# Kernel optimization log

Measured on AMD Instinct MI355X. Metric: run time of the kernel, lower is better.

The kernel has to match this reference:

```python
import jax, jax.numpy as jnp
import numpy as np

N = 50000      # total nodes
E = 800000     # total edges
IN = 8         # in_channels
H = 16         # hidden_dim
OUT = 16       # out_channels
B = 64         # number of graphs in batch


def _glorot(k, shape):
    fan_out, fan_in = shape[0], shape[1]
    lim = float(np.sqrt(6.0 / (fan_in + fan_out)))
    return jax.random.uniform(k, shape, jnp.float32, -lim, lim)


def setup_inputs() -> dict:
    key = jax.random.key(0)
    ks = jax.random.split(key, 12)
    return {
        "x": jax.random.normal(ks[0], (N, IN), jnp.float32),
        "edge_attr": jax.random.uniform(ks[1], (E, 1), jnp.float32),
        # edge MLP 1: Linear(1, H) -> ReLU -> Linear(H, IN*H)
        "W_e1a": _glorot(ks[2], (H, 1)), "b_e1a": jnp.zeros((H,), jnp.float32),
        "W_e1b": _glorot(ks[3], (IN * H, H)), "b_e1b": jnp.zeros((IN * H,), jnp.float32),
        "root1": _glorot(ks[4], (IN, H)), "bias1": jnp.zeros((H,), jnp.float32),
        # edge MLP 2: Linear(1, H) -> ReLU -> Linear(H, H*OUT)
        "W_e2a": _glorot(ks[5], (H, 1)), "b_e2a": jnp.zeros((H,), jnp.float32),
        "W_e2b": _glorot(ks[6], (H * OUT, H)), "b_e2b": jnp.zeros((H * OUT,), jnp.float32),
        "root2": _glorot(ks[7], (H, OUT)), "bias2": jnp.zeros((OUT,), jnp.float32),
        "edge_index": jax.random.randint(ks[8], (2, E), 0, N, jnp.int32),
        "batch": jnp.sort(jax.random.randint(ks[9], (N,), 0, B, jnp.int32)),
    }


def _segment_mean(vals, idx, num_segments):
    s = jax.ops.segment_sum(vals, idx, num_segments=num_segments)
    cnt = jax.ops.segment_sum(jnp.ones((vals.shape[0],), vals.dtype), idx,
                              num_segments=num_segments)
    return s / jnp.maximum(cnt, 1.0)[:, None]


def _nnconv(x, src, dst, edge_attr, Wa, ba, Wb, bb, root, bias, din, dout):
    # edge MLP -> per-edge weight matrix [E, din, dout]
    he = jax.nn.relu(edge_attr @ Wa.T + ba)
    We = (he @ Wb.T + bb).reshape(-1, din, dout)
    # per-edge matmul on gathered source features, scatter-mean to dst
    msg = jnp.einsum('ei,eio->eo', x[src], We)
    agg = _segment_mean(msg, dst, x.shape[0])
    return agg + x @ root + bias


def reference(x, edge_attr, W_e1a, b_e1a, W_e1b, b_e1b, root1, bias1,
              W_e2a, b_e2a, W_e2b, b_e2b, root2, bias2, edge_index, batch):
    src, dst = edge_index[0], edge_index[1]
    h = jax.nn.relu(_nnconv(x, src, dst, edge_attr,
                            W_e1a, b_e1a, W_e1b, b_e1b, root1, bias1, IN, H))
    h = jax.nn.relu(_nnconv(h, src, dst, edge_attr,
                            W_e2a, b_e2a, W_e2b, b_e2b, root2, bias2, H, OUT))
    g = _segment_mean(h, batch, B)  # global mean pool per graph
    return (h, g, batch)
```

## Files before the change

### kernel.cpp

```cpp
#include <hip/hip_runtime.h>
#include <hip/hip_bf16.h>

typedef __bf16 bf16;
typedef __bf16 bf16x8 __attribute__((ext_vector_type(8)));
typedef float  f32x4  __attribute__((ext_vector_type(4)));


__global__ void node_pre1(const float* __restrict__ x,
                          const float* __restrict__ b_e1b,
                          const float* __restrict__ root1,
                          const float* __restrict__ bias1,
                          float* __restrict__ d1, float* __restrict__ r1, int N)
{
    int t = blockIdx.x * blockDim.x + threadIdx.x;
    int v = t >> 4, o = t & 15;
    if (v >= N) return;
    float dacc = 0.f, racc = 0.f;
#pragma unroll
    for (int i = 0; i < 8; ++i) {
        float xv = x[v * 8 + i];
        dacc += xv * b_e1b[i * 16 + o];
        racc += xv * root1[i * 16 + o];
    }
    d1[v * 16 + o] = dacc;
    r1[v * 16 + o] = racc + bias1[o];
}

__global__ void edge_l1(const float* __restrict__ x,
                        const float* __restrict__ ea,
                        const int*   __restrict__ eidx,
                        const float* __restrict__ W_e1a, const float* __restrict__ b_e1a,
                        const float* __restrict__ W_e1b,
                        const float* __restrict__ d1,
                        float* __restrict__ agg, int* __restrict__ cnt,
                        int E, int ntiles)
{
    const int lane = threadIdx.x & 63;
    const int m = lane & 15;
    const int q = lane >> 4;
    const int wave   = blockIdx.x * (blockDim.x >> 6) + (threadIdx.x >> 6);
    const int nwaves = gridDim.x * (blockDim.x >> 6);

    bf16x8 bfrag[4];
#pragma unroll
    for (int c = 0; c < 4; ++c)
#pragma unroll
        for (int t = 0; t < 8; ++t)
            bfrag[c][t] = (bf16)W_e1b[(t * 16 + m) * 16 + (c * 4 + q)];

    float wa[4], bb[4];
#pragma unroll
    for (int c = 0; c < 4; ++c) { wa[c] = W_e1a[c * 4 + q]; bb[c] = b_e1a[c * 4 + q]; }

    int tile = wave;
    if (tile >= ntiles) return;

    int e = tile * 16 + m;
    int s = eidx[e];
    int d = eidx[E + e];
    float t_ea = ea[e];

    while (tile < ntiles) {
        const int ntile = tile + nwaves;
        int s_nx = s, d_nx = d; float ea_nx = t_ea;
        if (ntile < ntiles) {
            int en = ntile * 16 + m;
            s_nx  = eidx[en];
            d_nx  = eidx[E + en];
            ea_nx = ea[en];
        }

        const float4* xp = (const float4*)(x + (size_t)s * 8);
        float4 x0 = xp[0], x1 = xp[1];

        int d_r[4];
        f32x4 acc;
#pragma unroll
        for (int reg = 0; reg < 4; ++reg) {
            int r = q * 4 + reg;
            int s_r = __shfl(s, r, 64);
            d_r[reg] = __shfl(d, r, 64);
            acc[reg] = d1[s_r * 16 + m];
        }

        float he[4];
#pragma unroll
        for (int c = 0; c < 4; ++c) {
            float h = wa[c] * t_ea + bb[c];
            he[c] = h > 0.f ? h : 0.f;
        }

        float xv[8] = {x0.x, x0.y, x0.z, x0.w, x1.x, x1.y, x1.z, x1.w};
#pragma unroll
        for (int c = 0; c < 4; ++c) {
            bf16x8 afrag;
#pragma unroll
            for (int t = 0; t < 8; ++t) afrag[t] = (bf16)(he[c] * xv[t]);
            acc = __builtin_amdgcn_mfma_f32_16x16x32_bf16(afrag, bfrag[c], acc, 0, 0, 0);
        }

        if (q == 0) atomicAdd(&cnt[d], 1);

#pragma unroll
        for (int reg = 0; reg < 4; ++reg)
            atomicAdd(&agg[d_r[reg] * 16 + m], acc[reg]);

        s = s_nx; d = d_nx; t_ea = ea_nx; tile = ntile;
    }
}

__global__ void node_fin1(const float* __restrict__ agg, const int* __restrict__ cnt,
                          const float* __restrict__ r1,
                          const float* __restrict__ b_e2b, const float* __restrict__ root2,
                          const float* __restrict__ bias2,
                          float* __restrict__ h1, float* __restrict__ d2,
                          float* __restrict__ r2, int N)
{
    int t = blockIdx.x * blockDim.x + threadIdx.x;
    int v = t >> 4, o = t & 15;
    if (v >= N) return;
    float c = (float)cnt[v]; c = c > 1.f ? c : 1.f;
    float h = agg[v * 16 + o] / c + r1[v * 16 + o];
    h = h > 0.f ? h : 0.f;
    h1[v * 16 + o] = h;
    float dacc = 0.f, racc = 0.f;
#pragma unroll
    for (int i = 0; i < 16; ++i) {
        float hv = __shfl(h, i, 16);
        dacc += hv * b_e2b[i * 16 + o];
        racc += hv * root2[i * 16 + o];
    }
    d2[v * 16 + o] = dacc;
    r2[v * 16 + o] = racc + bias2[o];
}

__global__ void edge_l2(const float* __restrict__ h1g,
                        const float* __restrict__ ea,
                        const int*   __restrict__ eidx,
                        const float* __restrict__ W_e2a, const float* __restrict__ b_e2a,
                        const float* __restrict__ W_e2b,
                        const float* __restrict__ d2,
                        float* __restrict__ agg, int E, int ntiles)
{
    const int lane = threadIdx.x & 63;
    const int m = lane & 15;
    const int q = lane >> 4;
    const int qh = q >> 1;
    const int ql = q & 1;
    const int wave   = blockIdx.x * (blockDim.x >> 6) + (threadIdx.x >> 6);
    const int nwaves = gridDim.x * (blockDim.x >> 6);

    bf16x8 bfrag[8];
#pragma unroll
    for (int c = 0; c < 8; ++c) {
        int j = c * 2 + qh;
#pragma unroll
        for (int t = 0; t < 8; ++t) {
            int i = ql * 8 + t;
            bfrag[c][t] = (bf16)W_e2b[(i * 16 + m) * 16 + j];
        }
    }

    float wa[8], bb[8];
#pragma unroll
    for (int c = 0; c < 8; ++c) { wa[c] = W_e2a[c * 2 + qh]; bb[c] = b_e2a[c * 2 + qh]; }

    int tile = wave;
    if (tile >= ntiles) return;

    int e = tile * 16 + m;
    int s = eidx[e];
    int d = eidx[E + e];
    float t_ea = ea[e];

    while (tile < ntiles) {
        const int ntile = tile + nwaves;
        int s_nx = s, d_nx = d; float ea_nx = t_ea;
        if (ntile < ntiles) {
            int en = ntile * 16 + m;
            s_nx  = eidx[en];
            d_nx  = eidx[E + en];
            ea_nx = ea[en];
        }

        const float4* hp = (const float4*)(h1g + (size_t)s * 16 + ql * 8);
        float4 h0 = hp[0], h1v = hp[1];

        int d_r[4];
        f32x4 acc;
#pragma unroll
        for (int reg = 0; reg < 4; ++reg) {
            int r = q * 4 + reg;
            int s_r = __shfl(s, r, 64);
            d_r[reg] = __shfl(d, r, 64);
            acc[reg] = d2[s_r * 16 + m];
        }

        float he[8];
#pragma unroll
        for (int c = 0; c < 8; ++c) {
            float h = wa[c] * t_ea + bb[c];
            he[c] = h > 0.f ? h : 0.f;
        }

        float hv[8] = {h0.x, h0.y, h0.z, h0.w, h1v.x, h1v.y, h1v.z, h1v.w};
#pragma unroll
        for (int c = 0; c < 8; ++c) {
            bf16x8 afrag;
#pragma unroll
            for (int t = 0; t < 8; ++t) afrag[t] = (bf16)(he[c] * hv[t]);
            acc = __builtin_amdgcn_mfma_f32_16x16x32_bf16(afrag, bfrag[c], acc, 0, 0, 0);
        }

#pragma unroll
        for (int reg = 0; reg < 4; ++reg)
            atomicAdd(&agg[d_r[reg] * 16 + m], acc[reg]);

        s = s_nx; d = d_nx; t_ea = ea_nx; tile = ntile;
    }
}

__global__ void node_fin2(const float* __restrict__ agg, const int* __restrict__ cnt,
                          const float* __restrict__ r2, const int* __restrict__ batch,
                          float* __restrict__ out_h, float* __restrict__ out_b, int N)
{
    int t = blockIdx.x * blockDim.x + threadIdx.x;
    int v = t >> 4, o = t & 15;
    if (v >= N) return;
    float c = (float)cnt[v]; c = c > 1.f ? c : 1.f;
    float h = agg[v * 16 + o] / c + r2[v * 16 + o];
    h = h > 0.f ? h : 0.f;
    out_h[v * 16 + o] = h;
    if (o == 0) out_b[v] = (float)batch[v];
}

__global__ void pool_seg(const float* __restrict__ h, const int* __restrict__ batch,
                         float* __restrict__ out_g, int N)
{
    const int b = blockIdx.x;
    int lo = 0, hi = N;
    while (lo < hi) { int mid = (lo + hi) >> 1; if (batch[mid] < b) lo = mid + 1; else hi = mid; }
    const int start = lo;
    hi = N;
    while (lo < hi) { int mid = (lo + hi) >> 1; if (batch[mid] < b + 1) lo = mid + 1; else hi = mid; }
    const int end = lo;

    const int ch = threadIdx.x & 15, grp = threadIdx.x >> 4;
    float acc = 0.f;
    for (int v = start + grp; v < end; v += 16)
        acc += h[(size_t)v * 16 + ch];

    __shared__ float red[256];
    red[threadIdx.x] = acc;
    __syncthreads();
#pragma unroll
    for (int s = 128; s >= 16; s >>= 1) {
        if (threadIdx.x < s) red[threadIdx.x] += red[threadIdx.x + s];
        __syncthreads();
    }
    if (threadIdx.x < 16) {
        float c = (float)(end - start); c = c > 1.f ? c : 1.f;
        out_g[b * 16 + threadIdx.x] = red[threadIdx.x] / c;
    }
}

extern "C" void kernel_launch(void* const* d_in, const int* in_sizes, int n_in,
                              void* d_out, int out_size, void* d_ws, size_t ws_size,
                              hipStream_t stream)
{
    const float* x     = (const float*)d_in[0];
    const float* ea    = (const float*)d_in[1];
    const float* W_e1a = (const float*)d_in[2];
    const float* b_e1a = (const float*)d_in[3];
    const float* W_e1b = (const float*)d_in[4];
    const float* b_e1b = (const float*)d_in[5];
    const float* root1 = (const float*)d_in[6];
    const float* bias1 = (const float*)d_in[7];
    const float* W_e2a = (const float*)d_in[8];
    const float* b_e2a = (const float*)d_in[9];
    const float* W_e2b = (const float*)d_in[10];
    const float* b_e2b = (const float*)d_in[11];
    const float* root2 = (const float*)d_in[12];
    const float* bias2 = (const float*)d_in[13];
    const int*   eidx  = (const int*)d_in[14];
    const int*   batch = (const int*)d_in[15];

    const int E  = in_sizes[1];
    const int N  = in_sizes[15];
    const int Bg = (out_size - N * 16 - N) / 16;

    char* ws = (char*)d_ws;
    size_t off = 0;
    int*   cnt  = (int*)(ws + off);   off += (size_t)N * 4;
    float* agg1 = (float*)(ws + off); off += (size_t)N * 16 * 4;
    float* agg2 = (float*)(ws + off); off += (size_t)N * 16 * 4;
    size_t zero_bytes = off;
    float* h1 = (float*)(ws + off); off += (size_t)N * 16 * 4;
    float* d1 = (float*)(ws + off); off += (size_t)N * 16 * 4;
    float* r1 = (float*)(ws + off); off += (size_t)N * 16 * 4;
    float* d2 = (float*)(ws + off); off += (size_t)N * 16 * 4;
    float* r2 = (float*)(ws + off); off += (size_t)N * 16 * 4;

    hipMemsetAsync(d_ws, 0, zero_bytes, stream);

    int nodeBlocks = (N * 16 + 255) / 256;
    int ntiles = E / 16;
    int edgeBlocks = 2048;

    node_pre1<<<nodeBlocks, 256, 0, stream>>>(x, b_e1b, root1, bias1, d1, r1, N);
    edge_l1<<<edgeBlocks, 256, 0, stream>>>(x, ea, eidx, W_e1a, b_e1a, W_e1b, d1,
                                            agg1, cnt, E, ntiles);
    node_fin1<<<nodeBlocks, 256, 0, stream>>>(agg1, cnt, r1, b_e2b, root2, bias2,
                                              h1, d2, r2, N);
    edge_l2<<<edgeBlocks, 256, 0, stream>>>(h1, ea, eidx, W_e2a, b_e2a, W_e2b, d2,
                                            agg2, E, ntiles);

    float* out_h = (float*)d_out;
    float* out_g = out_h + (size_t)N * 16;
    float* out_b = out_g + (size_t)Bg * 16;
    node_fin2<<<nodeBlocks, 256, 0, stream>>>(agg2, cnt, r2, batch, out_h,
                                              out_b, N);
    pool_seg<<<Bg, 256, 0, stream>>>(out_h, batch, out_g, N);
}
```

Before: 285.9 us.

## Replace atomic scatter-mean with CSR sort by destination and segmented reduction

Builds a CSR by destination each call using a degree histogram, a two-level scan and a scatter of (src, edge_attr) pairs. Both edge kernels now write per-edge messages contiguously to a buffer instead of doing float atomics on the aggregate. Per-node kernels then reduce each node's message range. This removes atomic contention and the count atomics, but adds five preprocessing kernels, atomic scatter, and a large message buffer (E*16 floats) written and read twice.

```diff
diff --git a/kernel.cpp b/kernel.cpp
--- a/kernel.cpp
+++ b/kernel.cpp
@@ -4,6 +4,73 @@
 typedef __bf16 bf16;
 typedef __bf16 bf16x8 __attribute__((ext_vector_type(8)));
 typedef float  f32x4  __attribute__((ext_vector_type(4)));
+
+
+
+__global__ void hist_deg(const int* __restrict__ eidx, int* __restrict__ deg, int E)
+{
+    int e = blockIdx.x * blockDim.x + threadIdx.x;
+    if (e < E) atomicAdd(&deg[eidx[E + e]], 1);
+}
+
+__global__ void scan_blocks(const int* __restrict__ deg, int* __restrict__ part,
+                            int* __restrict__ bsum, int N)
+{
+    __shared__ int sm[256];
+    const int t = threadIdx.x;
+    const int i = blockIdx.x * 256 + t;
+    int v = (i < N) ? deg[i] : 0;
+    sm[t] = v;
+    __syncthreads();
+#pragma unroll
+    for (int ofs = 1; ofs < 256; ofs <<= 1) {
+        int add = (t >= ofs) ? sm[t - ofs] : 0;
+        __syncthreads();
+        sm[t] += add;
+        __syncthreads();
+    }
+    if (i < N) part[i] = sm[t] - v;
+    if (t == 255) bsum[blockIdx.x] = sm[255];
+}
+
+__global__ void scan_top(const int* __restrict__ bsum, int* __restrict__ boff, int nb)
+{
+    __shared__ int sm[256];
+    const int t = threadIdx.x;
+    int v = (t < nb) ? bsum[t] : 0;
+    sm[t] = v;
+    __syncthreads();
+#pragma unroll
+    for (int ofs = 1; ofs < 256; ofs <<= 1) {
+        int add = (t >= ofs) ? sm[t - ofs] : 0;
+        __syncthreads();
+        sm[t] += add;
+        __syncthreads();
+    }
+    if (t < nb) boff[t] = sm[t] - v;
+}
+
+__global__ void scan_fix(int* __restrict__ rowptr, int* __restrict__ cursor,
+                         const int* __restrict__ boff, int N, int E)
+{
+    int i = blockIdx.x * 256 + threadIdx.x;
+    if (i < N) {
+        int r = rowptr[i] + boff[blockIdx.x];
+        rowptr[i] = r;
+        cursor[i] = r;
+    }
+    if (i == N) rowptr[N] = E;
+}
+
+__global__ void scatter_edges(const int* __restrict__ eidx, const float* __restrict__ ea,
+                              int* __restrict__ cursor, int2* __restrict__ edat, int E)
+{
+    int e = blockIdx.x * blockDim.x + threadIdx.x;
+    if (e >= E) return;
+    int d = eidx[E + e];
+    int j = atomicAdd(&cursor[d], 1);
+    edat[j] = make_int2(eidx[e], __float_as_int(ea[e]));
+}
 
 
 __global__ void node_pre1(const float* __restrict__ x,
@@ -27,13 +94,11 @@
 }
 
 __global__ void edge_l1(const float* __restrict__ x,
-                        const float* __restrict__ ea,
-                        const int*   __restrict__ eidx,
+                        const int2*  __restrict__ edat,
                         const float* __restrict__ W_e1a, const float* __restrict__ b_e1a,
                         const float* __restrict__ W_e1b,
                         const float* __restrict__ d1,
-                        float* __restrict__ agg, int* __restrict__ cnt,
-                        int E, int ntiles)
+                        float* __restrict__ msg, int ntiles)
 {
     const int lane = threadIdx.x & 63;
     const int m = lane & 15;
@@ -55,31 +120,23 @@
     int tile = wave;
     if (tile >= ntiles) return;
 
-    int e = tile * 16 + m;
-    int s = eidx[e];
-    int d = eidx[E + e];
-    float t_ea = ea[e];
+    int2 ed = edat[tile * 16 + m];
 
     while (tile < ntiles) {
         const int ntile = tile + nwaves;
-        int s_nx = s, d_nx = d; float ea_nx = t_ea;
-        if (ntile < ntiles) {
-            int en = ntile * 16 + m;
-            s_nx  = eidx[en];
-            d_nx  = eidx[E + en];
-            ea_nx = ea[en];
-        }
+        int2 ed_nx = ed;
+        if (ntile < ntiles) ed_nx = edat[ntile * 16 + m];
+
+        const int s = ed.x;
+        const float t_ea = __int_as_float(ed.y);
 
         const float4* xp = (const float4*)(x + (size_t)s * 8);
         float4 x0 = xp[0], x1 = xp[1];
 
-        int d_r[4];
         f32x4 acc;
 #pragma unroll
         for (int reg = 0; reg < 4; ++reg) {
-            int r = q * 4 + reg;
-            int s_r = __shfl(s, r, 64);
-            d_r[reg] = __shfl(d, r, 64);
+            int s_r = __shfl(s, q * 4 + reg, 64);
             acc[reg] = d1[s_r * 16 + m];
         }
 
@@ -99,28 +156,31 @@
             acc = __builtin_amdgcn_mfma_f32_16x16x32_bf16(afrag, bfrag[c], acc, 0, 0, 0);
         }
 
-        if (q == 0) atomicAdd(&cnt[d], 1);
-
+        float* mrow = msg + (size_t)tile * 256;
 #pragma unroll
         for (int reg = 0; reg < 4; ++reg)
-            atomicAdd(&agg[d_r[reg] * 16 + m], acc[reg]);
-
-        s = s_nx; d = d_nx; t_ea = ea_nx; tile = ntile;
-    }
-}
-
-__global__ void node_fin1(const float* __restrict__ agg, const int* __restrict__ cnt,
-                          const float* __restrict__ r1,
-                          const float* __restrict__ b_e2b, const float* __restrict__ root2,
-                          const float* __restrict__ bias2,
-                          float* __restrict__ h1, float* __restrict__ d2,
-                          float* __restrict__ r2, int N)
+            mrow[(q * 4 + reg) * 16 + m] = acc[reg];
+
+        ed = ed_nx; tile = ntile;
+    }
+}
+
+__global__ void agg_fin1(const float* __restrict__ msg, const int* __restrict__ rowptr,
+                         const float* __restrict__ r1,
+                         const float* __restrict__ b_e2b, const float* __restrict__ root2,
+                         const float* __restrict__ bias2,
+                         float* __restrict__ h1, float* __restrict__ d2,
+                         float* __restrict__ r2, int N)
 {
     int t = blockIdx.x * blockDim.x + threadIdx.x;
     int v = t >> 4, o = t & 15;
     if (v >= N) return;
-    float c = (float)cnt[v]; c = c > 1.f ? c : 1.f;
-    float h = agg[v * 16 + o] / c + r1[v * 16 + o];
+    int j0 = rowptr[v], j1 = rowptr[v + 1];
+    float acc = 0.f;
+    for (int j = j0; j < j1; ++j)
+        acc += msg[(size_t)j * 16 + o];
+    float c = (float)(j1 - j0); c = c > 1.f ? c : 1.f;
+    float h = acc / c + r1[v * 16 + o];
     h = h > 0.f ? h : 0.f;
     h1[v * 16 + o] = h;
     float dacc = 0.f, racc = 0.f;
@@ -135,12 +195,11 @@
 }
 
 __global__ void edge_l2(const float* __restrict__ h1g,
-                        const float* __restrict__ ea,
-                        const int*   __restrict__ eidx,
+                        const int2*  __restrict__ edat,
                         const float* __restrict__ W_e2a, const float* __restrict__ b_e2a,
                         const float* __restrict__ W_e2b,
                         const float* __restrict__ d2,
-                        float* __restrict__ agg, int E, int ntiles)
+                        float* __restrict__ msg, int ntiles)
 {
     const int lane = threadIdx.x & 63;
     const int m = lane & 15;
@@ -168,31 +227,23 @@
     int tile = wave;
     if (tile >= ntiles) return;
 
-    int e = tile * 16 + m;
-    int s = eidx[e];
-    int d = eidx[E + e];
-    float t_ea = ea[e];
+    int2 ed = edat[tile * 16 + m];
 
     while (tile < ntiles) {
         const int ntile = tile + nwaves;
-        int s_nx = s, d_nx = d; float ea_nx = t_ea;
-        if (ntile < ntiles) {
-            int en = ntile * 16 + m;
-            s_nx  = eidx[en];
-            d_nx  = eidx[E + en];
-            ea_nx = ea[en];
-        }
+        int2 ed_nx = ed;
+        if (ntile < ntiles) ed_nx = edat[ntile * 16 + m];
+
+        const int s = ed.x;
+        const float t_ea = __int_as_float(ed.y);
 
         const float4* hp = (const float4*)(h1g + (size_t)s * 16 + ql * 8);
         float4 h0 = hp[0], h1v = hp[1];
 
-        int d_r[4];
         f32x4 acc;
 #pragma unroll
         for (int reg = 0; reg < 4; ++reg) {
-            int r = q * 4 + reg;
-            int s_r = __shfl(s, r, 64);
-            d_r[reg] = __shfl(d, r, 64);
+            int s_r = __shfl(s, q * 4 + reg, 64);
             acc[reg] = d2[s_r * 16 + m];
         }
 
@@ -212,23 +263,28 @@
             acc = __builtin_amdgcn_mfma_f32_16x16x32_bf16(afrag, bfrag[c], acc, 0, 0, 0);
         }
 
+        float* mrow = msg + (size_t)tile * 256;
 #pragma unroll
         for (int reg = 0; reg < 4; ++reg)
-            atomicAdd(&agg[d_r[reg] * 16 + m], acc[reg]);
-
-        s = s_nx; d = d_nx; t_ea = ea_nx; tile = ntile;
-    }
-}
-
-__global__ void node_fin2(const float* __restrict__ agg, const int* __restrict__ cnt,
-                          const float* __restrict__ r2, const int* __restrict__ batch,
-                          float* __restrict__ out_h, float* __restrict__ out_b, int N)
+            mrow[(q * 4 + reg) * 16 + m] = acc[reg];
+
+        ed = ed_nx; tile = ntile;
+    }
+}
+
+__global__ void agg_fin2(const float* __restrict__ msg, const int* __restrict__ rowptr,
+                         const float* __restrict__ r2, const int* __restrict__ batch,
+                         float* __restrict__ out_h, float* __restrict__ out_b, int N)
 {
     int t = blockIdx.x * blockDim.x + threadIdx.x;
     int v = t >> 4, o = t & 15;
     if (v >= N) return;
-    float c = (float)cnt[v]; c = c > 1.f ? c : 1.f;
-    float h = agg[v * 16 + o] / c + r2[v * 16 + o];
+    int j0 = rowptr[v], j1 = rowptr[v + 1];
+    float acc = 0.f;
+    for (int j = j0; j < j1; ++j)
+        acc += msg[(size_t)j * 16 + o];
+    float c = (float)(j1 - j0); c = c > 1.f ? c : 1.f;
+    float h = acc / c + r2[v * 16 + o];
     h = h > 0.f ? h : 0.f;
     out_h[v * 16 + o] = h;
     if (o == 0) out_b[v] = (float)batch[v];
@@ -289,36 +345,51 @@
     const int N  = in_sizes[15];
     const int Bg = (out_size - N * 16 - N) / 16;
 
+    auto align16 = [](size_t v) { return (v + 15) & ~(size_t)15; };
+
     char* ws = (char*)d_ws;
     size_t off = 0;
-    int*   cnt  = (int*)(ws + off);   off += (size_t)N * 4;
-    float* agg1 = (float*)(ws + off); off += (size_t)N * 16 * 4;
-    float* agg2 = (float*)(ws + off); off += (size_t)N * 16 * 4;
+    int*   deg    = (int*)(ws + off);  off = align16(off + (size_t)N * 4);
     size_t zero_bytes = off;
-    float* h1 = (float*)(ws + off); off += (size_t)N * 16 * 4;
-    float* d1 = (float*)(ws + off); off += (size_t)N * 16 * 4;
-    float* r1 = (float*)(ws + off); off += (size_t)N * 16 * 4;
-    float* d2 = (float*)(ws + off); off += (size_t)N * 16 * 4;
-    float* r2 = (float*)(ws + off); off += (size_t)N * 16 * 4;
+    int*   rowptr = (int*)(ws + off);  off = align16(off + (size_t)(N + 1) * 4);
+    int*   cursor = (int*)(ws + off);  off = align16(off + (size_t)N * 4);
+    int*   bsum   = (int*)(ws + off);  off = align16(off + 256 * 4);
+    int*   boff   = (int*)(ws + off);  off = align16(off + 256 * 4);
+    int2*  edat   = (int2*)(ws + off); off = align16(off + (size_t)E * 8);
+    float* msg    = (float*)(ws + off); off = align16(off + (size_t)E * 16 * 4);
+    float* d1 = (float*)(ws + off); off = align16(off + (size_t)N * 16 * 4);
+    float* r1 = (float*)(ws + off); off = align16(off + (size_t)N * 16 * 4);
+    float* h1 = (float*)(ws + off); off = align16(off + (size_t)N * 16 * 4);
+    float* d2 = (float*)(ws + off); off = align16(off + (size_t)N * 16 * 4);
+    float* r2 = (float*)(ws + off); off = align16(off + (size_t)N * 16 * 4);
 
     hipMemsetAsync(d_ws, 0, zero_bytes, stream);
 
-    int nodeBlocks = (N * 16 + 255) / 256;
-    int ntiles = E / 16;
-    int edgeBlocks = 2048;
+    const int nodeBlocks = (N * 16 + 255) / 256;
+    const int edgeThreadBlocks = (E + 255) / 256;
+    const int scanBlocks = (N + 255) / 256;
+    const int ntiles = E / 16;
+    const int edgeBlocks = 2048;
+
+    hist_deg<<<edgeThreadBlocks, 256, 0, stream>>>(eidx, deg, E);
+    scan_blocks<<<scanBlocks, 256, 0, stream>>>(deg, rowptr, bsum, N);
+    scan_top<<<1, 256, 0, stream>>>(bsum, boff, scanBlocks);
+    scan_fix<<<scanBlocks, 256, 0, stream>>>(rowptr, cursor, boff, N, E);
+    scatter_edges<<<edgeThreadBlocks, 256, 0, stream>>>(eidx, ea, cursor, edat, E);
 
     node_pre1<<<nodeBlocks, 256, 0, stream>>>(x, b_e1b, root1, bias1, d1, r1, N);
-    edge_l1<<<edgeBlocks, 256, 0, stream>>>(x, ea, eidx, W_e1a, b_e1a, W_e1b, d1,
-                                            agg1, cnt, E, ntiles);
-    node_fin1<<<nodeBlocks, 256, 0, stream>>>(agg1, cnt, r1, b_e2b, root2, bias2,
-                                              h1, d2, r2, N);
-    edge_l2<<<edgeBlocks, 256, 0, stream>>>(h1, ea, eidx, W_e2a, b_e2a, W_e2b, d2,
-                                            agg2, E, ntiles);
+    edge_l1<<<edgeBlocks, 256, 0, stream>>>(x, edat, W_e1a, b_e1a, W_e1b, d1,
+                                            msg, ntiles);
+    agg_fin1<<<nodeBlocks, 256, 0, stream>>>(msg, rowptr, r1, b_e2b, root2, bias2,
+                                             h1, d2, r2, N);
+
+    edge_l2<<<edgeBlocks, 256, 0, stream>>>(h1, edat, W_e2a, b_e2a, W_e2b, d2,
+                                            msg, ntiles);
 
     float* out_h = (float*)d_out;
     float* out_g = out_h + (size_t)N * 16;
     float* out_b = out_g + (size_t)Bg * 16;
-    node_fin2<<<nodeBlocks, 256, 0, stream>>>(agg2, cnt, r2, batch, out_h,
-                                              out_b, N);
+    agg_fin2<<<nodeBlocks, 256, 0, stream>>>(msg, rowptr, r2, batch, out_h,
+                                             out_b, N);
     pool_seg<<<Bg, 256, 0, stream>>>(out_h, batch, out_g, N);
 }
```

After: 373.4 us. 30.6% more time.

## Fold edge-MLP output bias into MFMA and fuse final node pass with pooling

Applied to the files above, without the earlier changes.

Computes the bias term of the edge MLP inside the edge kernels as an extra MFMA against a bias B-fragment, removing the node_pre1 kernel and the per-edge gathers of the precomputed d1/d2 arrays. The root1 projection moves into node_fin1, and node_fin2 is fused with the global mean pool via atomics into a pooled sum plus a last-block ticket that finalizes the outputs. Edge index and attribute loads become nontemporal. This saves a kernel launch and scattered gathers at the cost of one extra MFMA per tile and float atomics on pool sums, which may contend.

```diff
diff --git a/kernel.cpp b/kernel.cpp
--- a/kernel.cpp
+++ b/kernel.cpp
@@ -5,33 +5,12 @@
 typedef __bf16 bf16x8 __attribute__((ext_vector_type(8)));
 typedef float  f32x4  __attribute__((ext_vector_type(4)));
 
-
-__global__ void node_pre1(const float* __restrict__ x,
-                          const float* __restrict__ b_e1b,
-                          const float* __restrict__ root1,
-                          const float* __restrict__ bias1,
-                          float* __restrict__ d1, float* __restrict__ r1, int N)
-{
-    int t = blockIdx.x * blockDim.x + threadIdx.x;
-    int v = t >> 4, o = t & 15;
-    if (v >= N) return;
-    float dacc = 0.f, racc = 0.f;
-#pragma unroll
-    for (int i = 0; i < 8; ++i) {
-        float xv = x[v * 8 + i];
-        dacc += xv * b_e1b[i * 16 + o];
-        racc += xv * root1[i * 16 + o];
-    }
-    d1[v * 16 + o] = dacc;
-    r1[v * 16 + o] = racc + bias1[o];
-}
 
 __global__ void edge_l1(const float* __restrict__ x,
                         const float* __restrict__ ea,
                         const int*   __restrict__ eidx,
                         const float* __restrict__ W_e1a, const float* __restrict__ b_e1a,
-                        const float* __restrict__ W_e1b,
-                        const float* __restrict__ d1,
+                        const float* __restrict__ W_e1b, const float* __restrict__ b_e1b,
                         float* __restrict__ agg, int* __restrict__ cnt,
                         int E, int ntiles)
 {
@@ -48,6 +27,11 @@
         for (int t = 0; t < 8; ++t)
             bfrag[c][t] = (bf16)W_e1b[(t * 16 + m) * 16 + (c * 4 + q)];
 
+    bf16x8 bfragb;
+#pragma unroll
+    for (int t = 0; t < 8; ++t)
+        bfragb[t] = (q == 0) ? (bf16)b_e1b[t * 16 + m] : (bf16)0.f;
+
     float wa[4], bb[4];
 #pragma unroll
     for (int c = 0; c < 4; ++c) { wa[c] = W_e1a[c * 4 + q]; bb[c] = b_e1a[c * 4 + q]; }
@@ -56,32 +40,28 @@
     if (tile >= ntiles) return;
 
     int e = tile * 16 + m;
-    int s = eidx[e];
-    int d = eidx[E + e];
-    float t_ea = ea[e];
+    int s = __builtin_nontemporal_load(eidx + e);
+    int d = __builtin_nontemporal_load(eidx + E + e);
+    float t_ea = __builtin_nontemporal_load(ea + e);
 
     while (tile < ntiles) {
         const int ntile = tile + nwaves;
         int s_nx = s, d_nx = d; float ea_nx = t_ea;
         if (ntile < ntiles) {
             int en = ntile * 16 + m;
-            s_nx  = eidx[en];
-            d_nx  = eidx[E + en];
-            ea_nx = ea[en];
+            s_nx  = __builtin_nontemporal_load(eidx + en);
+            d_nx  = __builtin_nontemporal_load(eidx + E + en);
+            ea_nx = __builtin_nontemporal_load(ea + en);
         }
 
         const float4* xp = (const float4*)(x + (size_t)s * 8);
         float4 x0 = xp[0], x1 = xp[1];
+        float xv[8] = {x0.x, x0.y, x0.z, x0.w, x1.x, x1.y, x1.z, x1.w};
 
         int d_r[4];
-        f32x4 acc;
-#pragma unroll
-        for (int reg = 0; reg < 4; ++reg) {
-            int r = q * 4 + reg;
-            int s_r = __shfl(s, r, 64);
-            d_r[reg] = __shfl(d, r, 64);
-            acc[reg] = d1[s_r * 16 + m];
-        }
+#pragma unroll
+        for (int reg = 0; reg < 4; ++reg)
+            d_r[reg] = __shfl(d, q * 4 + reg, 64);
 
         float he[4];
 #pragma unroll
@@ -90,7 +70,13 @@
             he[c] = h > 0.f ? h : 0.f;
         }
 
-        float xv[8] = {x0.x, x0.y, x0.z, x0.w, x1.x, x1.y, x1.z, x1.w};
+        f32x4 acc = {0.f, 0.f, 0.f, 0.f};
+        {
+            bf16x8 afb;
+#pragma unroll
+            for (int t = 0; t < 8; ++t) afb[t] = (bf16)xv[t];
+            acc = __builtin_amdgcn_mfma_f32_16x16x32_bf16(afb, bfragb, acc, 0, 0, 0);
+        }
 #pragma unroll
         for (int c = 0; c < 4; ++c) {
             bf16x8 afrag;
@@ -110,36 +96,34 @@
 }
 
 __global__ void node_fin1(const float* __restrict__ agg, const int* __restrict__ cnt,
-                          const float* __restrict__ r1,
-                          const float* __restrict__ b_e2b, const float* __restrict__ root2,
-                          const float* __restrict__ bias2,
-                          float* __restrict__ h1, float* __restrict__ d2,
-                          float* __restrict__ r2, int N)
+                          const float* __restrict__ x,
+                          const float* __restrict__ root1, const float* __restrict__ bias1,
+                          const float* __restrict__ root2, const float* __restrict__ bias2,
+                          float* __restrict__ h1, float* __restrict__ r2, int N)
 {
     int t = blockIdx.x * blockDim.x + threadIdx.x;
     int v = t >> 4, o = t & 15;
     if (v >= N) return;
+    float r1v = bias1[o];
+#pragma unroll
+    for (int i = 0; i < 8; ++i)
+        r1v += x[v * 8 + i] * root1[i * 16 + o];
     float c = (float)cnt[v]; c = c > 1.f ? c : 1.f;
-    float h = agg[v * 16 + o] / c + r1[v * 16 + o];
+    float h = agg[v * 16 + o] / c + r1v;
     h = h > 0.f ? h : 0.f;
     h1[v * 16 + o] = h;
-    float dacc = 0.f, racc = 0.f;
-#pragma unroll
-    for (int i = 0; i < 16; ++i) {
-        float hv = __shfl(h, i, 16);
-        dacc += hv * b_e2b[i * 16 + o];
-        racc += hv * root2[i * 16 + o];
-    }
-    d2[v * 16 + o] = dacc;
-    r2[v * 16 + o] = racc + bias2[o];
+    float racc = bias2[o];
+#pragma unroll
+    for (int i = 0; i < 16; ++i)
+        racc += __shfl(h, i, 16) * root2[i * 16 + o];
+    r2[v * 16 + o] = racc;
 }
 
 __global__ void edge_l2(const float* __restrict__ h1g,
                         const float* __restrict__ ea,
                         const int*   __restrict__ eidx,
                         const float* __restrict__ W_e2a, const float* __restrict__ b_e2a,
-                        const float* __restrict__ W_e2b,
-                        const float* __restrict__ d2,
+                        const float* __restrict__ W_e2b, const float* __restrict__ b_e2b,
                         float* __restrict__ agg, int E, int ntiles)
 {
     const int lane = threadIdx.x & 63;
@@ -161,6 +145,11 @@
         }
     }
 
+    bf16x8 bfragb;
+#pragma unroll
+    for (int t = 0; t < 8; ++t)
+        bfragb[t] = (qh == 0) ? (bf16)b_e2b[(ql * 8 + t) * 16 + m] : (bf16)0.f;
+
     float wa[8], bb[8];
 #pragma unroll
     for (int c = 0; c < 8; ++c) { wa[c] = W_e2a[c * 2 + qh]; bb[c] = b_e2a[c * 2 + qh]; }
@@ -169,32 +158,28 @@
     if (tile >= ntiles) return;
 
     int e = tile * 16 + m;
-    int s = eidx[e];
-    int d = eidx[E + e];
-    float t_ea = ea[e];
+    int s = __builtin_nontemporal_load(eidx + e);
+    int d = __builtin_nontemporal_load(eidx + E + e);
+    float t_ea = __builtin_nontemporal_load(ea + e);
 
     while (tile < ntiles) {
         const int ntile = tile + nwaves;
         int s_nx = s, d_nx = d; float ea_nx = t_ea;
         if (ntile < ntiles) {
             int en = ntile * 16 + m;
-            s_nx  = eidx[en];
-            d_nx  = eidx[E + en];
-            ea_nx = ea[en];
+            s_nx  = __builtin_nontemporal_load(eidx + en);
+            d_nx  = __builtin_nontemporal_load(eidx + E + en);
+            ea_nx = __builtin_nontemporal_load(ea + en);
         }
 
         const float4* hp = (const float4*)(h1g + (size_t)s * 16 + ql * 8);
         float4 h0 = hp[0], h1v = hp[1];
+        float hv[8] = {h0.x, h0.y, h0.z, h0.w, h1v.x, h1v.y, h1v.z, h1v.w};
 
         int d_r[4];
-        f32x4 acc;
-#pragma unroll
-        for (int reg = 0; reg < 4; ++reg) {
-            int r = q * 4 + reg;
-            int s_r = __shfl(s, r, 64);
-            d_r[reg] = __shfl(d, r, 64);
-            acc[reg] = d2[s_r * 16 + m];
-        }
+#pragma unroll
+        for (int reg = 0; reg < 4; ++reg)
+            d_r[reg] = __shfl(d, q * 4 + reg, 64);
 
         float he[8];
 #pragma unroll
@@ -203,7 +188,13 @@
             he[c] = h > 0.f ? h : 0.f;
         }
 
-        float hv[8] = {h0.x, h0.y, h0.z, h0.w, h1v.x, h1v.y, h1v.z, h1v.w};
+        f32x4 acc = {0.f, 0.f, 0.f, 0.f};
+        {
+            bf16x8 afb;
+#pragma unroll
+            for (int t = 0; t < 8; ++t) afb[t] = (bf16)hv[t];
+            acc = __builtin_amdgcn_mfma_f32_16x16x32_bf16(afb, bfragb, acc, 0, 0, 0);
+        }
 #pragma unroll
         for (int c = 0; c < 8; ++c) {
             bf16x8 afrag;
@@ -220,47 +211,60 @@
     }
 }
 
-__global__ void node_fin2(const float* __restrict__ agg, const int* __restrict__ cnt,
-                          const float* __restrict__ r2, const int* __restrict__ batch,
-                          float* __restrict__ out_h, float* __restrict__ out_b, int N)
-{
-    int t = blockIdx.x * blockDim.x + threadIdx.x;
-    int v = t >> 4, o = t & 15;
-    if (v >= N) return;
-    float c = (float)cnt[v]; c = c > 1.f ? c : 1.f;
-    float h = agg[v * 16 + o] / c + r2[v * 16 + o];
-    h = h > 0.f ? h : 0.f;
-    out_h[v * 16 + o] = h;
-    if (o == 0) out_b[v] = (float)batch[v];
-}
-
-__global__ void pool_seg(const float* __restrict__ h, const int* __restrict__ batch,
-                         float* __restrict__ out_g, int N)
-{
-    const int b = blockIdx.x;
-    int lo = 0, hi = N;
-    while (lo < hi) { int mid = (lo + hi) >> 1; if (batch[mid] < b) lo = mid + 1; else hi = mid; }
-    const int start = lo;
-    hi = N;
-    while (lo < hi) { int mid = (lo + hi) >> 1; if (batch[mid] < b + 1) lo = mid + 1; else hi = mid; }
-    const int end = lo;
-
-    const int ch = threadIdx.x & 15, grp = threadIdx.x >> 4;
-    float acc = 0.f;
-    for (int v = start + grp; v < end; v += 16)
-        acc += h[(size_t)v * 16 + ch];
-
-    __shared__ float red[256];
-    red[threadIdx.x] = acc;
+__global__ void node_fin2_pool(const float* __restrict__ agg, const int* __restrict__ cnt,
+                               const float* __restrict__ r2, const int* __restrict__ batch,
+                               float* __restrict__ out_h, float* __restrict__ out_b,
+                               float* __restrict__ poolsum, int* __restrict__ done,
+                               float* __restrict__ out_g, int N, int Bg)
+{
+    const int t = blockIdx.x * blockDim.x + threadIdx.x;
+    const int v = t >> 4, o = t & 15;
+    const int lane = threadIdx.x & 63;
+    const int q = lane >> 4;
+
+    float h = 0.f; int b = 0;
+    const bool valid = v < N;
+    if (valid) {
+        float c = (float)cnt[v]; c = c > 1.f ? c : 1.f;
+        h = agg[v * 16 + o] / c + r2[v * 16 + o];
+        h = h > 0.f ? h : 0.f;
+        out_h[(size_t)v * 16 + o] = h;
+        if (o == 0) out_b[v] = (float)batch[v];
+        b = batch[v];
+    }
+
+    unsigned long long vb = __ballot(valid);
+    int b0 = __shfl(b, 0, 64);
+    if (vb == ~0ULL && __all(b == b0)) {
+        h += __shfl_xor(h, 16, 64);
+        h += __shfl_xor(h, 32, 64);
+        if (q == 0) atomicAdd(&poolsum[b * 16 + o], h);
+    } else if (valid) {
+        atomicAdd(&poolsum[b * 16 + o], h);
+    }
+
+    __shared__ int lastflag;
+    __shared__ int gstart[257];
     __syncthreads();
-#pragma unroll
-    for (int s = 128; s >= 16; s >>= 1) {
-        if (threadIdx.x < s) red[threadIdx.x] += red[threadIdx.x + s];
-        __syncthreads();
-    }
-    if (threadIdx.x < 16) {
-        float c = (float)(end - start); c = c > 1.f ? c : 1.f;
-        out_g[b * 16 + threadIdx.x] = red[threadIdx.x] / c;
+    if (threadIdx.x == 0) {
+        __threadfence();
+        int tkt = atomicAdd(done, 1);
+        lastflag = (tkt == (int)gridDim.x - 1) ? 1 : 0;
+    }
+    __syncthreads();
+    if (!lastflag) return;
+
+    for (int g = threadIdx.x; g <= Bg; g += blockDim.x) {
+        int lo = 0, hi = N;
+        while (lo < hi) { int mid = (lo + hi) >> 1; if (batch[mid] < g) lo = mid + 1; else hi = mid; }
+        gstart[g] = lo;
+    }
+    __syncthreads();
+    for (int idx = threadIdx.x; idx < Bg * 16; idx += blockDim.x) {
+        int g = idx >> 4;
+        float cg = (float)(gstart[g + 1] - gstart[g]); cg = cg > 1.f ? cg : 1.f;
+        float sv = atomicAdd(&poolsum[idx], 0.f);
+        out_g[idx] = sv / cg;
     }
 }
 
@@ -289,36 +293,36 @@
     const int N  = in_sizes[15];
     const int Bg = (out_size - N * 16 - N) / 16;
 
+    auto align16 = [](size_t v) { return (v + 15) & ~(size_t)15; };
+
     char* ws = (char*)d_ws;
     size_t off = 0;
-    int*   cnt  = (int*)(ws + off);   off += (size_t)N * 4;
-    float* agg1 = (float*)(ws + off); off += (size_t)N * 16 * 4;
-    float* agg2 = (float*)(ws + off); off += (size_t)N * 16 * 4;
+    int*   cnt     = (int*)(ws + off);   off = align16(off + (size_t)N * 4);
+    float* agg1    = (float*)(ws + off); off = align16(off + (size_t)N * 16 * 4);
+    float* agg2    = (float*)(ws + off); off = align16(off + (size_t)N * 16 * 4);
+    float* poolsum = (float*)(ws + off); off = align16(off + (size_t)Bg * 16 * 4);
+    int*   done    = (int*)(ws + off);   off = align16(off + 16);
     size_t zero_bytes = off;
-    float* h1 = (float*)(ws + off); off += (size_t)N * 16 * 4;
-    float* d1 = (float*)(ws + off); off += (size_t)N * 16 * 4;
-    float* r1 = (float*)(ws + off); off += (size_t)N * 16 * 4;
-    float* d2 = (float*)(ws + off); off += (size_t)N * 16 * 4;
-    float* r2 = (float*)(ws + off); off += (size_t)N * 16 * 4;
+    float* h1 = (float*)(ws + off); off = align16(off + (size_t)N * 16 * 4);
+    float* r2 = (float*)(ws + off); off = align16(off + (size_t)N * 16 * 4);
 
     hipMemsetAsync(d_ws, 0, zero_bytes, stream);
 
-    int nodeBlocks = (N * 16 + 255) / 256;
-    int ntiles = E / 16;
-    int edgeBlocks = 2048;
-
-    node_pre1<<<nodeBlocks, 256, 0, stream>>>(x, b_e1b, root1, bias1, d1, r1, N);
-    edge_l1<<<edgeBlocks, 256, 0, stream>>>(x, ea, eidx, W_e1a, b_e1a, W_e1b, d1,
-                                            agg1, cnt, E, ntiles);
-    node_fin1<<<nodeBlocks, 256, 0, stream>>>(agg1, cnt, r1, b_e2b, root2, bias2,
-                                              h1, d2, r2, N);
-    edge_l2<<<edgeBlocks, 256, 0, stream>>>(h1, ea, eidx, W_e2a, b_e2a, W_e2b, d2,
-                                            agg2, E, ntiles);
+    const int nodeBlocks = (N * 16 + 255) / 256;
+    const int ntiles = E / 16;
+    const int edgeBlocks = 2048;
+
+    edge_l1<<<edgeBlocks, 256, 0, stream>>>(x, ea, eidx, W_e1a, b_e1a,
+                                            W_e1b, b_e1b, agg1, cnt, E, ntiles);
+    node_fin1<<<nodeBlocks, 256, 0, stream>>>(agg1, cnt, x, root1, bias1,
+                                              root2, bias2, h1, r2, N);
+    edge_l2<<<edgeBlocks, 256, 0, stream>>>(h1, ea, eidx, W_e2a, b_e2a,
+                                            W_e2b, b_e2b, agg2, E, ntiles);
 
     float* out_h = (float*)d_out;
     float* out_g = out_h + (size_t)N * 16;
     float* out_b = out_g + (size_t)Bg * 16;
-    node_fin2<<<nodeBlocks, 256, 0, stream>>>(agg2, cnt, r2, batch, out_h,
-                                              out_b, N);
-    pool_seg<<<Bg, 256, 0, stream>>>(out_h, batch, out_g, N);
-}
+    node_fin2_pool<<<nodeBlocks, 256, 0, stream>>>(agg2, cnt, r2, batch,
+                                                   out_h, out_b, poolsum, done,
+                                                   out_g, N, Bg);
+}
```

Result: slower. 349.2 us (+22.1%).
